# Kernel optimization log

Hardware: AMD Instinct MI355X
Metric: run time of the kernel (lower is better)

The kernel has to match this reference:

```python
import jax, jax.numpy as jnp
import numpy as np

B, S, D = 4, 2048, 128

def _phi(x, W, d):
    # original: phi(x) = (1/sqrt(M)) * exp(-0.5*||x||_2) * exp(W @ x), M = d
    proj = jnp.exp(jnp.einsum('...d,md->...m', x, W))          # [..., d]
    scale = jnp.exp(-0.5 * jnp.linalg.norm(x, axis=-1, keepdims=True))
    return (scale / jnp.sqrt(jnp.asarray(d, x.dtype))) * proj

def setup_inputs() -> dict:
    key = jax.random.key(0)
    k1, k2, k3, k4 = jax.random.split(key, 4)
    # scale 0.1 keeps exp(W @ x) well within fp32 range
    K = jax.random.normal(k1, (B, S, D), dtype=jnp.float32) * 0.1
    Q = jax.random.normal(k2, (B, S, D), dtype=jnp.float32) * 0.1
    V = jax.random.normal(k3, (B, S, D), dtype=jnp.float32) * 0.1
    W_phi = jax.random.normal(k4, (D, D), dtype=jnp.float32)
    sent_embed_slice = jnp.zeros((B, 1), dtype=jnp.float32)
    return {"K": K, "Q": Q, "V": V, "sent_embed_slice": sent_embed_slice,
            "max_seq_length": S, "qkv_size": D, "W_phi": W_phi}

def reference(K, Q, V, sent_embed_slice, max_seq_length, qkv_size, W_phi):
    d = qkv_size
    phiK = _phi(K, W_phi, d)   # [B, S, d]
    phiQ = _phi(Q, W_phi, d)   # [B, S, d]
    Bn = K.shape[0]

    def step(carry, inp):
        Mst, Nst = carry                       # [B, d, d], [B, d]
        pk, v, pq = inp                        # each [B, d]
        Mst = Mst + pk[:, :, None] * v[:, None, :]   # cumulative outer product
        Nst = Nst + pk                               # cumulative feature sum
        num = jnp.einsum('bd,bde->be', pq, Mst)      # phi(q) @ M
        r = jnp.einsum('bd,bd->b', pq, Nst)          # phi(q) . N
        out = num / (r + jnp.sign(r) * 1e-6)[:, None]
        return (Mst, Nst), out

    init = (jnp.zeros((Bn, d, d), K.dtype), jnp.zeros((Bn, d), K.dtype))
    xs = (jnp.swapaxes(phiK, 0, 1), jnp.swapaxes(V, 0, 1), jnp.swapaxes(phiQ, 0, 1))
    _, outs = jax.lax.scan(step, init, xs)    # outs: [S, B, d]
    return jnp.swapaxes(outs, 0, 1)           # [B, S, d]
```

## Files before the change

### kernel.cpp

```cpp
#include <hip/hip_runtime.h>

typedef float v4 __attribute__((ext_vector_type(4)));
typedef short s8v __attribute__((ext_vector_type(8)));
typedef float f4v __attribute__((ext_vector_type(4)));
typedef unsigned short u16;
typedef u16 us4 __attribute__((ext_vector_type(4)));
typedef u16 us8 __attribute__((ext_vector_type(8)));

#define BN 4
#define SN 2048
#define DN 128

#define OFF_PHIKB 0
#define OFF_PHIQB 524288
#define OFF_KVT   1048576
#define OFF_N32   5242880
#define OFF_PMB   5275648
#define OFF_PN    7372800

__device__ inline u16 f2bf(float f) {
  union { float f; unsigned u; } v; v.f = f;
  unsigned r = v.u + 0x7fffu + ((v.u >> 16) & 1u);
  return (u16)(r >> 16);
}
__device__ inline float bf2f(u16 h) {
  union { unsigned u; float f; } v; v.u = ((unsigned)h) << 16; return v.f;
}

__global__ __launch_bounds__(256) void phi_kernel(
    const float* __restrict__ K, const float* __restrict__ Q,
    const float* __restrict__ W, u16* __restrict__ phiKb,
    u16* __restrict__ phiQb) {
  __shared__ float XT[32][68];
  __shared__ float WT[32][132];
  __shared__ float scl[64];

  const int tid = threadIdx.x;
  const float* X = blockIdx.y ? Q : K;
  u16* out = blockIdx.y ? phiQb : phiKb;
  const int row0 = blockIdx.x * 64;

  const int r0 = (tid >> 4) * 4;
  const int c0 = (tid & 15) * 4;

  float acc[4][8];
#pragma unroll
  for (int i = 0; i < 4; i++)
#pragma unroll
    for (int j = 0; j < 8; j++) acc[i][j] = 0.f;
  float sumsq = 0.f;

  for (int dc = 0; dc < 4; dc++) {
    __syncthreads();
#pragma unroll
    for (int k = 0; k < 2; k++) {
      int j = tid + k * 256;
      int r = j >> 3;
      int d0 = (j & 7) * 4;
      v4 x4 = *(const v4*)&X[(size_t)(row0 + r) * 128 + dc * 32 + d0];
      XT[d0 + 0][r] = x4[0]; XT[d0 + 1][r] = x4[1];
      XT[d0 + 2][r] = x4[2]; XT[d0 + 3][r] = x4[3];
    }
#pragma unroll
    for (int k = 0; k < 4; k++) {
      int j = tid + k * 256;
      int m = j >> 3;
      int d0 = (j & 7) * 4;
      v4 w4 = *(const v4*)&W[(size_t)m * 128 + dc * 32 + d0];
      WT[d0 + 0][m] = w4[0]; WT[d0 + 1][m] = w4[1];
      WT[d0 + 2][m] = w4[2]; WT[d0 + 3][m] = w4[3];
    }
    __syncthreads();
    if (tid < 64) {
#pragma unroll
      for (int dd = 0; dd < 32; dd++) { float v = XT[dd][tid]; sumsq += v * v; }
    }
#pragma unroll
    for (int d4 = 0; d4 < 8; d4++) {
      v4 xv[4], wv0[4], wv1[4];
#pragma unroll
      for (int k = 0; k < 4; k++) {
        int d = d4 * 4 + k;
        xv[k] = *(const v4*)&XT[d][r0];
        wv0[k] = *(const v4*)&WT[d][c0];
        wv1[k] = *(const v4*)&WT[d][c0 + 64];
      }
#pragma unroll
      for (int k = 0; k < 4; k++)
#pragma unroll
        for (int i = 0; i < 4; i++) {
          float x = xv[k][i];
#pragma unroll
          for (int j = 0; j < 4; j++) {
            acc[i][j] += x * wv0[k][j];
            acc[i][j + 4] += x * wv1[k][j];
          }
        }
    }
  }
  if (tid < 64) scl[tid] = 0.08838834764831845f * __expf(-0.5f * sqrtf(sumsq));
  __syncthreads();
#pragma unroll
  for (int i = 0; i < 4; i++) {
    float s = scl[r0 + i];
    us4 o0, o1;
#pragma unroll
    for (int j = 0; j < 4; j++) {
      o0[j] = f2bf(s * __expf(acc[i][j]));
      o1[j] = f2bf(s * __expf(acc[i][j + 4]));
    }
    *(us4*)&out[(size_t)(row0 + r0 + i) * 128 + c0] = o0;
    *(us4*)&out[(size_t)(row0 + r0 + i) * 128 + c0 + 64] = o1;
  }
}

__global__ __launch_bounds__(256) void kv_kernel(
    const u16* __restrict__ phiKb, const float* __restrict__ V,
    float* __restrict__ KVT, float* __restrict__ N32) {
  __shared__ float Ks[32][128];
  __shared__ float Vs[32][128];
  const int tid = threadIdx.x;
  const int b = blockIdx.x >> 6;
  const int c = blockIdx.x & 63;
  const int srow0 = b * 2048 + c * 32;

#pragma unroll
  for (int k = 0; k < 2; k++) {
    int j = tid + k * 256;
    int s = j >> 4;
    int d8 = (j & 15) * 8;
    us8 kk = *(const us8*)&phiKb[(size_t)(srow0 + s) * 128 + d8];
#pragma unroll
    for (int i = 0; i < 8; i++) Ks[s][d8 + i] = bf2f(kk[i]);
  }
#pragma unroll
  for (int k = 0; k < 4; k++) {
    int j = tid + k * 256;
    int s = j >> 5;
    int e4 = (j & 31) * 4;
    *(v4*)&Vs[s][e4] = *(const v4*)&V[(size_t)(srow0 + s) * 128 + e4];
  }
  __syncthreads();

  const int e0 = (tid >> 4) * 8;
  const int d0 = (tid & 15) * 4;
  float acc[8][8];
#pragma unroll
  for (int i = 0; i < 8; i++)
#pragma unroll
    for (int j = 0; j < 8; j++) acc[i][j] = 0.f;

#pragma unroll 4
  for (int s = 0; s < 32; s++) {
    v4 a0 = *(const v4*)&Vs[s][e0];
    v4 a1 = *(const v4*)&Vs[s][e0 + 4];
    v4 b0 = *(const v4*)&Ks[s][d0];
    v4 b1 = *(const v4*)&Ks[s][d0 + 64];
#pragma unroll
    for (int i = 0; i < 4; i++)
#pragma unroll
      for (int j = 0; j < 4; j++) {
        acc[i][j] += a0[i] * b0[j];
        acc[i][j + 4] += a0[i] * b1[j];
        acc[i + 4][j] += a1[i] * b0[j];
        acc[i + 4][j + 4] += a1[i] * b1[j];
      }
  }

  if (tid < 128) {
    float ns = 0.f;
#pragma unroll
    for (int s = 0; s < 32; s++) ns += Ks[s][tid];
    N32[(size_t)(b * 64 + c) * 128 + tid] = ns;
  }

  const size_t base = (size_t)(b * 64 + c) * (128 * 128);
#pragma unroll
  for (int i = 0; i < 8; i++) {
    v4 o0, o1;
#pragma unroll
    for (int j = 0; j < 4; j++) { o0[j] = acc[i][j]; o1[j] = acc[i][j + 4]; }
    *(v4*)&KVT[base + (size_t)(e0 + i) * 128 + d0] = o0;
    *(v4*)&KVT[base + (size_t)(e0 + i) * 128 + d0 + 64] = o1;
  }
}

__global__ __launch_bounds__(128) void prefix_kernel(
    const float* __restrict__ KVT, const float* __restrict__ N32,
    u16* __restrict__ PMb, float* __restrict__ PN) {
  const int tid = threadIdx.x;
  const int bid = blockIdx.x;
  if (bid < 512) {
    const int b = bid >> 7;
    const int e = bid & 127;
    const float* src = KVT + ((size_t)(b * 64) * 128 + e) * 128 + tid;
    u16* dst = PMb + ((size_t)(b * 64) * 128 + e) * 128 + tid;
    float acc = 0.f;
#pragma unroll 8
    for (int c = 0; c < 64; c++) {
      dst[(size_t)c * 16384] = f2bf(acc);
      acc += src[(size_t)c * 16384];
    }
  } else {
    const int b = bid - 512;
    float acc = 0.f;
#pragma unroll 8
    for (int c = 0; c < 64; c++) {
      PN[(size_t)(b * 64 + c) * 128 + tid] = acc;
      acc += N32[(size_t)(b * 64 + c) * 128 + tid];
    }
  }
}

__global__ __launch_bounds__(256) void out_kernel(
    const u16* __restrict__ phiKb, const u16* __restrict__ phiQb,
    const float* __restrict__ V, const u16* __restrict__ PMb,
    const float* __restrict__ PN, float* __restrict__ out) {
  __shared__ __align__(16) u16 Qs[32][136];
  __shared__ __align__(16) u16 Ms[128][136];
  __shared__ __align__(16) u16 KsVt[128 * 40];
  __shared__ __align__(16) u16 Ps[32][40];
  __shared__ float Ns[128];
  __shared__ float rs[32];

  const int tid = threadIdx.x;
  const int b = blockIdx.x >> 6;
  const int c = blockIdx.x & 63;
  const int srow0 = b * 2048 + c * 32;
  const int wave = tid >> 6;
  const int lane = tid & 63;
  const int q = lane >> 4;
  const int ln = lane & 15;

#pragma unroll
  for (int k = 0; k < 2; k++) {
    int j = tid + k * 256;
    int t = j >> 4;
    int d8 = (j & 15) * 8;
    *(us8*)&Qs[t][d8] = *(const us8*)&phiQb[(size_t)(srow0 + t) * 128 + d8];
    *(us8*)&KsVt[t * 136 + d8] =
        *(const us8*)&phiKb[(size_t)(srow0 + t) * 128 + d8];
  }
#pragma unroll
  for (int k = 0; k < 8; k++) {
    int j = tid + k * 256;
    int e = j >> 4;
    int d8 = (j & 15) * 8;
    *(us8*)&Ms[e][d8] =
        *(const us8*)&PMb[((size_t)(b * 64 + c) * 128 + e) * 128 + d8];
  }
  if (tid < 128) Ns[tid] = PN[(size_t)(b * 64 + c) * 128 + tid];
  __syncthreads();

  {
    const int tr = wave >> 1, tc = wave & 1;
    f4v acc = {0.f, 0.f, 0.f, 0.f};
#pragma unroll
    for (int ks = 0; ks < 4; ks++) {
      s8v a = *(const s8v*)&Qs[tr * 16 + ln][ks * 32 + q * 8];
      s8v bb = *(const s8v*)&KsVt[(tc * 16 + ln) * 136 + ks * 32 + q * 8];
      acc = __builtin_amdgcn_mfma_f32_16x16x32_bf16(a, bb, acc, 0, 0, 0);
    }
    const int s_g = tc * 16 + ln;
#pragma unroll
    for (int r = 0; r < 4; r++) {
      int t_g = tr * 16 + q * 4 + r;
      Ps[t_g][s_g] = f2bf(s_g <= t_g ? acc[r] : 0.f);
    }
  }
  __syncthreads();

#pragma unroll
  for (int k = 0; k < 4; k++) {
    int j = tid + k * 256;
    int s = j & 31;
    int e4 = (j >> 5) * 4;
    v4 vv = *(const v4*)&V[(size_t)(srow0 + s) * 128 + e4];
#pragma unroll
    for (int i = 0; i < 4; i++) KsVt[(e4 + i) * 40 + s] = f2bf(vv[i]);
  }
  {
    const int t = tid >> 3;
    const int p8 = tid & 7;
    float rsl = 0.f;
#pragma unroll
    for (int s = p8; s < 32; s += 8) rsl += bf2f(Ps[t][s]);
#pragma unroll
    for (int d = p8; d < 128; d += 8) rsl += bf2f(Qs[t][d]) * Ns[d];
    rsl += __shfl_down(rsl, 4, 8);
    rsl += __shfl_down(rsl, 2, 8);
    rsl += __shfl_down(rsl, 1, 8);
    if (p8 == 0) rs[t] = rsl;
  }
  __syncthreads();

  const int e0 = wave * 32;
  f4v acc2[2][2];
#pragma unroll
  for (int i = 0; i < 2; i++)
#pragma unroll
    for (int j = 0; j < 2; j++) acc2[i][j] = (f4v){0.f, 0.f, 0.f, 0.f};

#pragma unroll
  for (int tr2 = 0; tr2 < 2; tr2++) {
    s8v a_p = *(const s8v*)&Ps[tr2 * 16 + ln][q * 8];
#pragma unroll
    for (int tc2 = 0; tc2 < 2; tc2++) {
      s8v b_v = *(const s8v*)&KsVt[(e0 + tc2 * 16 + ln) * 40 + q * 8];
      acc2[tr2][tc2] =
          __builtin_amdgcn_mfma_f32_16x16x32_bf16(a_p, b_v, acc2[tr2][tc2], 0, 0, 0);
    }
  }
#pragma unroll
  for (int ks = 0; ks < 4; ks++) {
#pragma unroll
    for (int tr2 = 0; tr2 < 2; tr2++) {
      s8v a_q = *(const s8v*)&Qs[tr2 * 16 + ln][ks * 32 + q * 8];
#pragma unroll
      for (int tc2 = 0; tc2 < 2; tc2++) {
        s8v b_m = *(const s8v*)&Ms[e0 + tc2 * 16 + ln][ks * 32 + q * 8];
        acc2[tr2][tc2] =
            __builtin_amdgcn_mfma_f32_16x16x32_bf16(a_q, b_m, acc2[tr2][tc2], 0, 0, 0);
      }
    }
  }

#pragma unroll
  for (int tr2 = 0; tr2 < 2; tr2++) {
#pragma unroll
    for (int r = 0; r < 4; r++) {
      int t_g = tr2 * 16 + q * 4 + r;
      float rv = rs[t_g];
      float den = rv + (rv > 0.f ? 1e-6f : (rv < 0.f ? -1e-6f : 0.f));
      float inv = 1.f / den;
#pragma unroll
      for (int tc2 = 0; tc2 < 2; tc2++) {
        int e_g = e0 + tc2 * 16 + ln;
        out[(size_t)(srow0 + t_g) * 128 + e_g] = acc2[tr2][tc2][r] * inv;
      }
    }
  }
}

extern "C" void kernel_launch(void* const* d_in, const int* in_sizes, int n_in,
                              void* d_out, int out_size, void* d_ws,
                              size_t ws_size, hipStream_t stream) {
  (void)in_sizes; (void)n_in; (void)out_size; (void)ws_size;
  const float* K = (const float*)d_in[0];
  const float* Q = (const float*)d_in[1];
  const float* V = (const float*)d_in[2];
  const float* W = (const float*)d_in[6];
  float* out = (float*)d_out;
  float* ws = (float*)d_ws;

  u16* phiKb = (u16*)(ws + OFF_PHIKB);
  u16* phiQb = (u16*)(ws + OFF_PHIQB);
  float* KVT = ws + OFF_KVT;
  float* N32 = ws + OFF_N32;
  u16* PMb = (u16*)(ws + OFF_PMB);
  float* PN = ws + OFF_PN;

  phi_kernel<<<dim3(128, 2), 256, 0, stream>>>(K, Q, W, phiKb, phiQb);
  kv_kernel<<<256, 256, 0, stream>>>(phiKb, V, KVT, N32);
  prefix_kernel<<<516, 128, 0, stream>>>(KVT, N32, PMb, PN);
  out_kernel<<<256, 256, 0, stream>>>(phiKb, phiQb, V, PMb, PN, out);
}
```

Baseline: 105.7 us.

## Fuse phi and chunk KV into one MFMA kernel with bf16 chunk states

Merges the phi feature-map kernel and the per-chunk K^T V kernel into one launch. Both projections (X·W^T and V^T·phiK) move from scalar FP32 FMAs to bf16 MFMA instructions. Chunk KV states are stored as bf16 in an [b,e,chunk,d] layout, so the prefix scan reads contiguous rows and the intermediate traffic is halved. The cost is lower precision in phi inputs, W and the chunk states, plus scattered 2-byte stores of KV state.

```diff
diff --git a/kernel.cpp b/kernel.cpp
--- a/kernel.cpp
+++ b/kernel.cpp
@@ -7,16 +7,12 @@
 typedef u16 us4 __attribute__((ext_vector_type(4)));
 typedef u16 us8 __attribute__((ext_vector_type(8)));
 
-#define BN 4
-#define SN 2048
-#define DN 128
-
 #define OFF_PHIKB 0
 #define OFF_PHIQB 524288
-#define OFF_KVT   1048576
+#define OFF_KVTB  1048576
+#define OFF_PMB   3145728
 #define OFF_N32   5242880
-#define OFF_PMB   5275648
-#define OFF_PN    7372800
+#define OFF_PN    5275648
 
 __device__ inline u16 f2bf(float f) {
   union { float f; unsigned u; } v; v.f = f;
@@ -27,179 +23,162 @@
   union { unsigned u; float f; } v; v.u = ((unsigned)h) << 16; return v.f;
 }
 
-__global__ __launch_bounds__(256) void phi_kernel(
+__global__ __launch_bounds__(256) void phikv_kernel(
     const float* __restrict__ K, const float* __restrict__ Q,
-    const float* __restrict__ W, u16* __restrict__ phiKb,
-    u16* __restrict__ phiQb) {
-  __shared__ float XT[32][68];
-  __shared__ float WT[32][132];
+    const float* __restrict__ V, const float* __restrict__ W,
+    u16* __restrict__ phiKb, u16* __restrict__ phiQb,
+    u16* __restrict__ KVTb, float* __restrict__ N32) {
+  __shared__ __align__(16) u16 smem[27136];
+  __shared__ float srowsq[64];
   __shared__ float scl[64];
+  u16* Xb = smem;
+  u16* Wb = smem + 8704;
+  u16* Pb = smem;
+  u16* KdT = smem + 8704;
+  u16* Vt = smem + 17920;
 
   const int tid = threadIdx.x;
-  const float* X = blockIdx.y ? Q : K;
-  u16* out = blockIdx.y ? phiQb : phiKb;
+  const bool isK = (blockIdx.y == 0);
+  const float* X = isK ? K : Q;
+  u16* outPhi = isK ? phiKb : phiQb;
   const int row0 = blockIdx.x * 64;
-
-  const int r0 = (tid >> 4) * 4;
-  const int c0 = (tid & 15) * 4;
-
-  float acc[4][8];
-#pragma unroll
-  for (int i = 0; i < 4; i++)
-#pragma unroll
-    for (int j = 0; j < 8; j++) acc[i][j] = 0.f;
-  float sumsq = 0.f;
-
-  for (int dc = 0; dc < 4; dc++) {
-    __syncthreads();
-#pragma unroll
-    for (int k = 0; k < 2; k++) {
+  const int wv = tid >> 6;
+  const int lane = tid & 63;
+  const int q = lane >> 4;
+  const int ln = lane & 15;
+
+#pragma unroll
+  for (int k = 0; k < 8; k++) {
+    int j = tid + k * 256;
+    int r = j >> 5;
+    int c4 = (j & 31) * 4;
+    v4 x = *(const v4*)&X[(size_t)(row0 + r) * 128 + c4];
+    us4 xb;
+    float p = 0.f;
+#pragma unroll
+    for (int i = 0; i < 4; i++) { xb[i] = f2bf(x[i]); p += x[i] * x[i]; }
+    *(us4*)&Xb[r * 136 + c4] = xb;
+    p += __shfl_down(p, 16, 32);
+    p += __shfl_down(p, 8, 32);
+    p += __shfl_down(p, 4, 32);
+    p += __shfl_down(p, 2, 32);
+    p += __shfl_down(p, 1, 32);
+    if ((tid & 31) == 0) srowsq[r] = p;
+  }
+#pragma unroll
+  for (int k = 0; k < 16; k++) {
+    int j = tid + k * 256;
+    int r = j >> 5;
+    int c4 = (j & 31) * 4;
+    v4 w = *(const v4*)&W[(size_t)r * 128 + c4];
+    us4 wb;
+#pragma unroll
+    for (int i = 0; i < 4; i++) wb[i] = f2bf(w[i]);
+    *(us4*)&Wb[r * 136 + c4] = wb;
+  }
+  __syncthreads();
+  if (tid < 64)
+    scl[tid] = 0.08838834764831845f * __expf(-0.5f * sqrtf(srowsq[tid]));
+
+  f4v acc[8];
+#pragma unroll
+  for (int ct = 0; ct < 8; ct++) acc[ct] = (f4v){0.f, 0.f, 0.f, 0.f};
+#pragma unroll
+  for (int ks = 0; ks < 4; ks++) {
+    s8v a = *(const s8v*)&Xb[(wv * 16 + ln) * 136 + ks * 32 + q * 8];
+#pragma unroll
+    for (int ct = 0; ct < 8; ct++) {
+      s8v bb = *(const s8v*)&Wb[(ct * 16 + ln) * 136 + ks * 32 + q * 8];
+      acc[ct] = __builtin_amdgcn_mfma_f32_16x16x32_bf16(a, bb, acc[ct], 0, 0, 0);
+    }
+  }
+  __syncthreads();
+
+#pragma unroll
+  for (int ct = 0; ct < 8; ct++) {
+    us4 col;
+#pragma unroll
+    for (int r = 0; r < 4; r++) {
+      int row = wv * 16 + q * 4 + r;
+      u16 hv = f2bf(scl[row] * __expf(acc[ct][r]));
+      Pb[row * 136 + ct * 16 + ln] = hv;
+      col[r] = hv;
+    }
+    if (isK) *(us4*)&KdT[(ct * 16 + ln) * 72 + wv * 16 + q * 4] = col;
+  }
+  if (isK) {
+#pragma unroll
+    for (int k = 0; k < 8; k++) {
       int j = tid + k * 256;
-      int r = j >> 3;
-      int d0 = (j & 7) * 4;
-      v4 x4 = *(const v4*)&X[(size_t)(row0 + r) * 128 + dc * 32 + d0];
-      XT[d0 + 0][r] = x4[0]; XT[d0 + 1][r] = x4[1];
-      XT[d0 + 2][r] = x4[2]; XT[d0 + 3][r] = x4[3];
-    }
-#pragma unroll
-    for (int k = 0; k < 4; k++) {
-      int j = tid + k * 256;
-      int m = j >> 3;
-      int d0 = (j & 7) * 4;
-      v4 w4 = *(const v4*)&W[(size_t)m * 128 + dc * 32 + d0];
-      WT[d0 + 0][m] = w4[0]; WT[d0 + 1][m] = w4[1];
-      WT[d0 + 2][m] = w4[2]; WT[d0 + 3][m] = w4[3];
-    }
-    __syncthreads();
-    if (tid < 64) {
-#pragma unroll
-      for (int dd = 0; dd < 32; dd++) { float v = XT[dd][tid]; sumsq += v * v; }
-    }
-#pragma unroll
-    for (int d4 = 0; d4 < 8; d4++) {
-      v4 xv[4], wv0[4], wv1[4];
-#pragma unroll
-      for (int k = 0; k < 4; k++) {
-        int d = d4 * 4 + k;
-        xv[k] = *(const v4*)&XT[d][r0];
-        wv0[k] = *(const v4*)&WT[d][c0];
-        wv1[k] = *(const v4*)&WT[d][c0 + 64];
+      int s = j >> 5;
+      int e4 = (j & 31) * 4;
+      v4 vv = *(const v4*)&V[(size_t)(row0 + s) * 128 + e4];
+#pragma unroll
+      for (int i = 0; i < 4; i++) Vt[(e4 + i) * 72 + s] = f2bf(vv[i]);
+    }
+  }
+  __syncthreads();
+
+#pragma unroll
+  for (int k = 0; k < 4; k++) {
+    int j = tid + k * 256;
+    int r = j >> 4;
+    int d8 = (j & 15) * 8;
+    *(us8*)&outPhi[(size_t)(row0 + r) * 128 + d8] = *(const us8*)&Pb[r * 136 + d8];
+  }
+  if (!isK) return;
+
+  const int b = row0 >> 11;
+  const int cgB = (row0 >> 5) & 63;
+
+  {
+    int c = tid >> 7;
+    int d = tid & 127;
+    float ns = 0.f;
+#pragma unroll
+    for (int s = 0; s < 32; s++) ns += bf2f(KdT[d * 72 + c * 32 + s]);
+    N32[(size_t)(b * 64 + cgB + c) * 128 + d] = ns;
+  }
+
+#pragma unroll
+  for (int c = 0; c < 2; c++) {
+#pragma unroll
+    for (int ei = 0; ei < 2; ei++) {
+      const int et = wv * 2 + ei;
+      s8v a = *(const s8v*)&Vt[(et * 16 + ln) * 72 + c * 32 + q * 8];
+      f4v ac[8];
+#pragma unroll
+      for (int dt = 0; dt < 8; dt++) ac[dt] = (f4v){0.f, 0.f, 0.f, 0.f};
+#pragma unroll
+      for (int dt = 0; dt < 8; dt++) {
+        s8v bb = *(const s8v*)&KdT[(dt * 16 + ln) * 72 + c * 32 + q * 8];
+        ac[dt] = __builtin_amdgcn_mfma_f32_16x16x32_bf16(a, bb, ac[dt], 0, 0, 0);
       }
 #pragma unroll
-      for (int k = 0; k < 4; k++)
-#pragma unroll
-        for (int i = 0; i < 4; i++) {
-          float x = xv[k][i];
-#pragma unroll
-          for (int j = 0; j < 4; j++) {
-            acc[i][j] += x * wv0[k][j];
-            acc[i][j + 4] += x * wv1[k][j];
-          }
+      for (int dt = 0; dt < 8; dt++)
+#pragma unroll
+        for (int r = 0; r < 4; r++) {
+          int e = et * 16 + q * 4 + r;
+          int d = dt * 16 + ln;
+          KVTb[((size_t)(b * 128 + e) * 64 + (cgB + c)) * 128 + d] =
+              f2bf(ac[dt][r]);
         }
     }
   }
-  if (tid < 64) scl[tid] = 0.08838834764831845f * __expf(-0.5f * sqrtf(sumsq));
-  __syncthreads();
-#pragma unroll
-  for (int i = 0; i < 4; i++) {
-    float s = scl[r0 + i];
-    us4 o0, o1;
-#pragma unroll
-    for (int j = 0; j < 4; j++) {
-      o0[j] = f2bf(s * __expf(acc[i][j]));
-      o1[j] = f2bf(s * __expf(acc[i][j + 4]));
-    }
-    *(us4*)&out[(size_t)(row0 + r0 + i) * 128 + c0] = o0;
-    *(us4*)&out[(size_t)(row0 + r0 + i) * 128 + c0 + 64] = o1;
-  }
-}
-
-__global__ __launch_bounds__(256) void kv_kernel(
-    const u16* __restrict__ phiKb, const float* __restrict__ V,
-    float* __restrict__ KVT, float* __restrict__ N32) {
-  __shared__ float Ks[32][128];
-  __shared__ float Vs[32][128];
-  const int tid = threadIdx.x;
-  const int b = blockIdx.x >> 6;
-  const int c = blockIdx.x & 63;
-  const int srow0 = b * 2048 + c * 32;
-
-#pragma unroll
-  for (int k = 0; k < 2; k++) {
-    int j = tid + k * 256;
-    int s = j >> 4;
-    int d8 = (j & 15) * 8;
-    us8 kk = *(const us8*)&phiKb[(size_t)(srow0 + s) * 128 + d8];
-#pragma unroll
-    for (int i = 0; i < 8; i++) Ks[s][d8 + i] = bf2f(kk[i]);
-  }
-#pragma unroll
-  for (int k = 0; k < 4; k++) {
-    int j = tid + k * 256;
-    int s = j >> 5;
-    int e4 = (j & 31) * 4;
-    *(v4*)&Vs[s][e4] = *(const v4*)&V[(size_t)(srow0 + s) * 128 + e4];
-  }
-  __syncthreads();
-
-  const int e0 = (tid >> 4) * 8;
-  const int d0 = (tid & 15) * 4;
-  float acc[8][8];
-#pragma unroll
-  for (int i = 0; i < 8; i++)
-#pragma unroll
-    for (int j = 0; j < 8; j++) acc[i][j] = 0.f;
-
-#pragma unroll 4
-  for (int s = 0; s < 32; s++) {
-    v4 a0 = *(const v4*)&Vs[s][e0];
-    v4 a1 = *(const v4*)&Vs[s][e0 + 4];
-    v4 b0 = *(const v4*)&Ks[s][d0];
-    v4 b1 = *(const v4*)&Ks[s][d0 + 64];
-#pragma unroll
-    for (int i = 0; i < 4; i++)
-#pragma unroll
-      for (int j = 0; j < 4; j++) {
-        acc[i][j] += a0[i] * b0[j];
-        acc[i][j + 4] += a0[i] * b1[j];
-        acc[i + 4][j] += a1[i] * b0[j];
-        acc[i + 4][j + 4] += a1[i] * b1[j];
-      }
-  }
-
-  if (tid < 128) {
-    float ns = 0.f;
-#pragma unroll
-    for (int s = 0; s < 32; s++) ns += Ks[s][tid];
-    N32[(size_t)(b * 64 + c) * 128 + tid] = ns;
-  }
-
-  const size_t base = (size_t)(b * 64 + c) * (128 * 128);
-#pragma unroll
-  for (int i = 0; i < 8; i++) {
-    v4 o0, o1;
-#pragma unroll
-    for (int j = 0; j < 4; j++) { o0[j] = acc[i][j]; o1[j] = acc[i][j + 4]; }
-    *(v4*)&KVT[base + (size_t)(e0 + i) * 128 + d0] = o0;
-    *(v4*)&KVT[base + (size_t)(e0 + i) * 128 + d0 + 64] = o1;
-  }
 }
 
 __global__ __launch_bounds__(128) void prefix_kernel(
-    const float* __restrict__ KVT, const float* __restrict__ N32,
+    const u16* __restrict__ KVTb, const float* __restrict__ N32,
     u16* __restrict__ PMb, float* __restrict__ PN) {
   const int tid = threadIdx.x;
   const int bid = blockIdx.x;
   if (bid < 512) {
-    const int b = bid >> 7;
-    const int e = bid & 127;
-    const float* src = KVT + ((size_t)(b * 64) * 128 + e) * 128 + tid;
-    u16* dst = PMb + ((size_t)(b * 64) * 128 + e) * 128 + tid;
+    const size_t base = (size_t)bid * 64 * 128;
     float acc = 0.f;
 #pragma unroll 8
     for (int c = 0; c < 64; c++) {
-      dst[(size_t)c * 16384] = f2bf(acc);
-      acc += src[(size_t)c * 16384];
+      PMb[base + c * 128 + tid] = f2bf(acc);
+      acc += bf2f(KVTb[base + c * 128 + tid]);
     }
   } else {
     const int b = bid - 512;
@@ -247,7 +226,7 @@
     int e = j >> 4;
     int d8 = (j & 15) * 8;
     *(us8*)&Ms[e][d8] =
-        *(const us8*)&PMb[((size_t)(b * 64 + c) * 128 + e) * 128 + d8];
+        *(const us8*)&PMb[((size_t)(b * 128 + e) * 64 + c) * 128 + d8];
   }
   if (tid < 128) Ns[tid] = PN[(size_t)(b * 64 + c) * 128 + tid];
   __syncthreads();
@@ -355,13 +334,13 @@
 
   u16* phiKb = (u16*)(ws + OFF_PHIKB);
   u16* phiQb = (u16*)(ws + OFF_PHIQB);
-  float* KVT = ws + OFF_KVT;
+  u16* KVTb = (u16*)(ws + OFF_KVTB);
+  u16* PMb = (u16*)(ws + OFF_PMB);
   float* N32 = ws + OFF_N32;
-  u16* PMb = (u16*)(ws + OFF_PMB);
   float* PN = ws + OFF_PN;
 
-  phi_kernel<<<dim3(128, 2), 256, 0, stream>>>(K, Q, W, phiKb, phiQb);
-  kv_kernel<<<256, 256, 0, stream>>>(phiKb, V, KVT, N32);
-  prefix_kernel<<<516, 128, 0, stream>>>(KVT, N32, PMb, PN);
+  phikv_kernel<<<dim3(128, 2), 256, 0, stream>>>(K, Q, V, W, phiKb, phiQb,
+                                                 KVTb, N32);
+  prefix_kernel<<<516, 128, 0, stream>>>(KVTb, N32, PMb, PN);
   out_kernel<<<256, 256, 0, stream>>>(phiKb, phiQb, V, PMb, PN, out);
 }
```

Result: faster. 95.58 us (-9.5%).
